# Optimization experiments

Hardware: AMD Instinct MI355X
Metric: run time of the kernel (lower is better)

Reference implementation:

```python
import jax, jax.numpy as jnp
import numpy as np

DIM = 1024
HEADS = 16
HEAD_DIM = DIM // HEADS


def setup_inputs() -> dict:
    key = jax.random.key(0)
    k_x, k_qkv, k_ow, k_ob = jax.random.split(key, 4)
    x = jax.random.normal(k_x, (2, 2048, DIM), dtype=jnp.float32)
    # nn.Linear(dim, 3*dim, bias=False): weight shape [3*dim, dim], y = x @ W.T
    w_qkv = jax.random.normal(k_qkv, (3 * DIM, DIM), dtype=jnp.float32) * (DIM ** -0.5)
    # nn.Linear(dim, dim) with bias
    w_o = jax.random.normal(k_ow, (DIM, DIM), dtype=jnp.float32) * (DIM ** -0.5)
    b_o = jax.random.normal(k_ob, (DIM,), dtype=jnp.float32) * 0.02
    return {"x": x, "w_qkv": w_qkv, "w_o": w_o, "b_o": b_o}


def reference(x, w_qkv, w_o, b_o):
    b, n, _ = x.shape
    scale = DIM ** -0.5  # NOTE: source scales by full dim, not head dim
    # qkv projection: [b, n, 3*dim]
    qkv = jnp.einsum('bnd,ed->bne', x, w_qkv)
    # 'b n (qkv h d) -> qkv b h n d'
    qkv = qkv.reshape(b, n, 3, HEADS, HEAD_DIM)
    q = jnp.transpose(qkv[:, :, 0], (0, 2, 1, 3))  # [b, h, n, d]
    k = jnp.transpose(qkv[:, :, 1], (0, 2, 1, 3))
    v = jnp.transpose(qkv[:, :, 2], (0, 2, 1, 3))
    scores = jnp.einsum('bhqd,bhkd->bhqk', q, k) * scale  # [b, h, n, n]
    attn = jax.nn.softmax(scores, axis=-1)
    out = jnp.einsum('bhqk,bhkd->bhqd', attn, v)  # [b, h, n, d]
    out = jnp.transpose(out, (0, 2, 1, 3)).reshape(b, n, DIM)  # 'b h n d -> b n (h d)'
    out = jnp.einsum('bnd,ed->bne', out, w_o) + b_o
    return out
```

## Files before the change

### kernel.cpp

```cpp
#include <hip/hip_runtime.h>
#include <stdint.h>


#define DIM 1024
#define SEQ 2048
#define BATCH 2
#define ROWS 4096
#define RSTRIDE 3072

typedef __bf16 bf16_t;
typedef bf16_t bf16x4 __attribute__((ext_vector_type(4)));
typedef bf16_t bf16x8 __attribute__((ext_vector_type(8)));
typedef float f32x4 __attribute__((ext_vector_type(4)));
typedef short s16x4 __attribute__((ext_vector_type(4)));

__device__ __forceinline__ ushort f2bf(float f) {
    uint32_t u;
    __builtin_memcpy(&u, &f, 4);
    uint32_t r = (u + 0x7fffu + ((u >> 16) & 1u)) >> 16;
    return (ushort)r;
}

__device__ __forceinline__ void store_out(ushort* p, float v) { *p = f2bf(v); }
__device__ __forceinline__ void store_out(float* p, float v) { *p = v; }

__device__ __forceinline__ void gl_lds16(const void* g, void* l) {
    __builtin_amdgcn_global_load_lds(
        (const __attribute__((address_space(1))) void*)g,
        (__attribute__((address_space(3))) void*)l, 16, 0, 0);
}

__global__ __launch_bounds__(256) void cvt3_kernel(
    const float* __restrict__ x, const float* __restrict__ wq,
    const float* __restrict__ wo, ushort* __restrict__ dst) {
    size_t i = ((size_t)blockIdx.x * 256 + threadIdx.x) * 8;
    const size_t n_x = (size_t)ROWS * DIM;
    const size_t n_wq = (size_t)3 * DIM * DIM;
    const float* src;
    size_t off;
    if (i < n_x) {
        src = x; off = i;
    } else if (i < n_x + n_wq) {
        src = wq; off = i - n_x;
    } else {
        src = wo; off = i - n_x - n_wq;
    }
    float4 a = *(const float4*)(src + off);
    float4 b = *(const float4*)(src + off + 4);
    uint4 u;
    u.x = (uint)f2bf(a.x) | ((uint)f2bf(a.y) << 16);
    u.y = (uint)f2bf(a.z) | ((uint)f2bf(a.w) << 16);
    u.z = (uint)f2bf(b.x) | ((uint)f2bf(b.y) << 16);
    u.w = (uint)f2bf(b.z) | ((uint)f2bf(b.w) << 16);
    *(uint4*)(dst + i) = u;
}

template <typename OutT, int BN>
__global__ __launch_bounds__(256) void gemm_bt_kernel(
    const ushort* __restrict__ A, const ushort* __restrict__ B,
    const float* __restrict__ bias, OutT* __restrict__ C,
    int M, int N, int K) {
    constexpr int JN = BN / 32;
    __shared__ __align__(16) ushort sA[128 * 64];
    __shared__ __align__(16) ushort sB[BN * 64];

    const int tid = threadIdx.x;
    const int lane = tid & 63, w = tid >> 6;
    const int quad = lane >> 4, l15 = lane & 15;
    const int wm = (w >> 1) * 64, wn = (w & 1) * (BN / 2);
    const int bm = blockIdx.y, bn = blockIdx.x;

    f32x4 acc[4][JN];
#pragma unroll
    for (int i = 0; i < 4; i++)
#pragma unroll
        for (int j = 0; j < JN; j++) acc[i][j] = (f32x4){0.f, 0.f, 0.f, 0.f};

    const ushort* Abase = A + (size_t)(bm * 128) * K;
    const ushort* Bbase = B + (size_t)(bn * BN) * K;
    const int rd = lane >> 3, c8 = lane & 7;
    const int sw = l15 & 7;

    for (int kk = 0; kk < K; kk += 64) {
        __syncthreads();
#pragma unroll
        for (int t = 0; t < 4; t++) {
            int row = w * 32 + t * 8;
            gl_lds16(Abase + (size_t)(row + rd) * K + kk + ((c8 ^ rd) * 8),
                     sA + row * 64);
        }
#pragma unroll
        for (int t = 0; t < BN / 32; t++) {
            int row = w * 8 + t * 32;
            gl_lds16(Bbase + (size_t)(row + rd) * K + kk + ((c8 ^ rd) * 8),
                     sB + row * 64);
        }
        __syncthreads();

#pragma unroll
        for (int kh = 0; kh < 2; kh++) {
            bf16x8 af[4], bfr[JN];
#pragma unroll
            for (int i = 0; i < 4; i++)
                af[i] = *(const bf16x8*)((const bf16_t*)sA +
                        (wm + i * 16 + l15) * 64 + (((kh * 4 + quad) ^ sw) * 8));
#pragma unroll
            for (int j = 0; j < JN; j++)
                bfr[j] = *(const bf16x8*)((const bf16_t*)sB +
                        (wn + j * 16 + l15) * 64 + (((kh * 4 + quad) ^ sw) * 8));
#pragma unroll
            for (int i = 0; i < 4; i++)
#pragma unroll
                for (int j = 0; j < JN; j++)
                    acc[i][j] = __builtin_amdgcn_mfma_f32_16x16x32_bf16(
                        af[i], bfr[j], acc[i][j], 0, 0, 0);
        }
    }

#pragma unroll
    for (int i = 0; i < 4; i++)
#pragma unroll
        for (int j = 0; j < JN; j++) {
            int col = bn * BN + wn + j * 16 + l15;
            float bv = bias ? bias[col] : 0.f;
#pragma unroll
            for (int r = 0; r < 4; r++) {
                int row = bm * 128 + wm + i * 16 + quad * 4 + r;
                store_out(&C[(size_t)row * N + col], acc[i][j][r] + bv);
            }
        }
}

template <typename OutT>
__global__ __launch_bounds__(512) void gemm_bt8_kernel(
    const ushort* __restrict__ A, const ushort* __restrict__ B,
    const float* __restrict__ bias, OutT* __restrict__ C,
    int M, int N, int K) {
    __shared__ __align__(16) ushort sA[128 * 64];
    __shared__ __align__(16) ushort sB[128 * 64];

    const int tid = threadIdx.x;
    const int lane = tid & 63, w = tid >> 6;
    const int quad = lane >> 4, l15 = lane & 15;
    const int wm = (w >> 2) * 64, wn = (w & 3) * 32;
    const int bm = blockIdx.y, bn = blockIdx.x;

    f32x4 acc[4][2];
#pragma unroll
    for (int i = 0; i < 4; i++)
#pragma unroll
        for (int j = 0; j < 2; j++) acc[i][j] = (f32x4){0.f, 0.f, 0.f, 0.f};

    const ushort* Abase = A + (size_t)(bm * 128) * K;
    const ushort* Bbase = B + (size_t)(bn * 128) * K;
    const int rd = lane >> 3, c8 = lane & 7;
    const int sw = l15 & 7;

    for (int kk = 0; kk < K; kk += 64) {
        __syncthreads();
#pragma unroll
        for (int t = 0; t < 2; t++) {
            int row = w * 16 + t * 8;
            gl_lds16(Abase + (size_t)(row + rd) * K + kk + ((c8 ^ rd) * 8),
                     sA + row * 64);
            gl_lds16(Bbase + (size_t)(row + rd) * K + kk + ((c8 ^ rd) * 8),
                     sB + row * 64);
        }
        __syncthreads();

#pragma unroll
        for (int kh = 0; kh < 2; kh++) {
            bf16x8 af[4], bfr[2];
#pragma unroll
            for (int i = 0; i < 4; i++)
                af[i] = *(const bf16x8*)((const bf16_t*)sA +
                        (wm + i * 16 + l15) * 64 + (((kh * 4 + quad) ^ sw) * 8));
#pragma unroll
            for (int j = 0; j < 2; j++)
                bfr[j] = *(const bf16x8*)((const bf16_t*)sB +
                        (wn + j * 16 + l15) * 64 + (((kh * 4 + quad) ^ sw) * 8));
#pragma unroll
            for (int i = 0; i < 4; i++)
#pragma unroll
                for (int j = 0; j < 2; j++)
                    acc[i][j] = __builtin_amdgcn_mfma_f32_16x16x32_bf16(
                        af[i], bfr[j], acc[i][j], 0, 0, 0);
        }
    }

#pragma unroll
    for (int i = 0; i < 4; i++)
#pragma unroll
        for (int j = 0; j < 2; j++) {
            int col = bn * 128 + wn + j * 16 + l15;
            float bv = bias ? bias[col] : 0.f;
#pragma unroll
            for (int r = 0; r < 4; r++) {
                int row = bm * 128 + wm + i * 16 + quad * 4 + r;
                store_out(&C[(size_t)row * N + col], acc[i][j][r] + bv);
            }
        }
}

__global__ __launch_bounds__(512, 4) void flash_attn_kernel(
    const ushort* __restrict__ qkv, ushort* __restrict__ out) {
    __shared__ __align__(16) ushort sK[128 * 64];
    __shared__ __align__(16) ushort sVt[64 * 128];

    const int tid = threadIdx.x;
    const int lane = tid & 63, w = tid >> 6;
    const int quad = lane >> 4, l15 = lane & 15;
    const int sw = l15 & 7;
    const int qh = quad >> 1, q1 = quad & 1;
    const int bh = blockIdx.y, b = bh >> 4, h = bh & 15;
    const int q0 = blockIdx.x * 128;
    const ushort* qkvb = qkv + (size_t)b * SEQ * RSTRIDE + h * 64;

    const ushort* qrow = qkvb + (size_t)(q0 + w * 16 + l15) * RSTRIDE;
    const bf16x8 aq0 = *(const bf16x8*)(qrow + quad * 8);
    const bf16x8 aq1 = *(const bf16x8*)(qrow + 32 + quad * 8);

    const int krow = tid >> 3, kc8 = tid & 7;
    const int kdst = krow * 64 + ((kc8 ^ (krow & 7)) * 8);
    const int vrp = tid & 63, vc = tid >> 6;
    const int vch = vrp >> 2, vlo = vrp & 3;

    uint4 kreg0, kreg1, va, vb;
    {
        const ushort* kp0 = qkvb + (size_t)krow * RSTRIDE + DIM + kc8 * 8;
        kreg0 = *(const uint4*)kp0;
        kreg1 = *(const uint4*)(kp0 + (size_t)64 * RSTRIDE);
        const ushort* v0 = qkvb + (size_t)(2 * vrp) * RSTRIDE + 2 * DIM + vc * 8;
        va = *(const uint4*)v0;
        vb = *(const uint4*)(v0 + RSTRIDE);
    }

    f32x4 l_acc = (f32x4){0.f, 0.f, 0.f, 0.f};
    f32x4 o[4];
#pragma unroll
    for (int j = 0; j < 4; j++) o[j] = (f32x4){0.f, 0.f, 0.f, 0.f};

    s16x4 vones;
#pragma unroll
    for (int e = 0; e < 4; e++) vones[e] = (short)0x3F80;

    const float c_exp = 0.04508422f;

    uint* vt32 = (uint*)sVt;
    for (int kb = 0; kb < SEQ; kb += 128) {
        *(uint4*)(sK + kdst) = kreg0;
        *(uint4*)(sK + 64 * 64 + kdst) = kreg1;
        {
            int base = (vc * 8) * 64 + vlo;
            vt32[base + 0 * 64 + ((vch ^ 0) << 2)] = (va.x & 0xffffu) | (vb.x << 16);
            vt32[base + 1 * 64 + ((vch ^ 1) << 2)] = (va.x >> 16) | (vb.x & 0xffff0000u);
            vt32[base + 2 * 64 + ((vch ^ 2) << 2)] = (va.y & 0xffffu) | (vb.y << 16);
            vt32[base + 3 * 64 + ((vch ^ 3) << 2)] = (va.y >> 16) | (vb.y & 0xffff0000u);
            vt32[base + 4 * 64 + ((vch ^ 4) << 2)] = (va.z & 0xffffu) | (vb.z << 16);
            vt32[base + 5 * 64 + ((vch ^ 5) << 2)] = (va.z >> 16) | (vb.z & 0xffff0000u);
            vt32[base + 6 * 64 + ((vch ^ 6) << 2)] = (va.w & 0xffffu) | (vb.w << 16);
            vt32[base + 7 * 64 + ((vch ^ 7) << 2)] = (va.w >> 16) | (vb.w & 0xffff0000u);
        }
        __syncthreads();

        int nkb = (kb + 128 < SEQ) ? kb + 128 : kb;
        {
            const ushort* kp0 = qkvb + (size_t)(nkb + krow) * RSTRIDE + DIM + kc8 * 8;
            kreg0 = *(const uint4*)kp0;
            kreg1 = *(const uint4*)(kp0 + (size_t)64 * RSTRIDE);
            const ushort* v0 =
                qkvb + (size_t)(nkb + 2 * vrp) * RSTRIDE + 2 * DIM + vc * 8;
            va = *(const uint4*)v0;
            vb = *(const uint4*)(v0 + RSTRIDE);
        }

        f32x4 s[8];
#pragma unroll
        for (int j = 0; j < 8; j++) {
            const ushort* kp = sK + (j * 16 + l15) * 64;
            bf16x8 bk0 = *(const bf16x8*)(kp + ((quad ^ sw) * 8));
            bf16x8 bk1 = *(const bf16x8*)(kp + (((4 | quad) ^ sw) * 8));
            f32x4 z = (f32x4){0.f, 0.f, 0.f, 0.f};
            __builtin_amdgcn_s_setprio(1);
            z = __builtin_amdgcn_mfma_f32_16x16x32_bf16(bk0, aq0, z, 0, 0, 0);
            z = __builtin_amdgcn_mfma_f32_16x16x32_bf16(bk1, aq1, z, 0, 0, 0);
            __builtin_amdgcn_s_setprio(0);
            s[j] = z;
        }

        s16x4 pa[8];
#pragma unroll
        for (int j = 0; j < 8; j++) {
            bf16x4 t;
#pragma unroll
            for (int r = 0; r < 4; r++)
                t[r] = (bf16_t)__builtin_amdgcn_exp2f(s[j][r] * c_exp);
            pa[j] = __builtin_bit_cast(s16x4, t);
        }

        __builtin_amdgcn_s_setprio(1);
#pragma unroll
        for (int j = 0; j < 8; j++)
            l_acc = __builtin_amdgcn_mfma_f32_16x16x16bf16_1k(
                pa[j], vones, l_acc, 0, 0, 0);
        __builtin_amdgcn_s_setprio(0);

#pragma unroll
        for (int jd = 0; jd < 4; jd++) {
            const bf16_t* vp = (const bf16_t*)sVt + (jd * 16 + l15) * 128;
            __builtin_amdgcn_s_setprio(1);
#pragma unroll
            for (int j = 0; j < 8; j++) {
                int ch = 2 * j + qh;
                bf16x4 bv = *(const bf16x4*)(vp + ((ch ^ sw) * 8 + q1 * 4));
                o[jd] = __builtin_amdgcn_mfma_f32_16x16x16bf16_1k(
                    pa[j], __builtin_bit_cast(s16x4, bv), o[jd], 0, 0, 0);
            }
            __builtin_amdgcn_s_setprio(0);
        }
        __syncthreads();
    }

#pragma unroll
    for (int r = 0; r < 4; r++) {
        float inv = 1.f / l_acc[r];
        int qrow_i = q0 + w * 16 + quad * 4 + r;
#pragma unroll
        for (int j = 0; j < 4; j++) {
            out[(size_t)(b * SEQ + qrow_i) * DIM + h * 64 + j * 16 + l15] =
                f2bf(o[j][r] * inv);
        }
    }
}

extern "C" void kernel_launch(void* const* d_in, const int* in_sizes, int n_in,
                              void* d_out, int out_size, void* d_ws, size_t ws_size,
                              hipStream_t stream) {
    const float* x = (const float*)d_in[0];
    const float* w_qkv = (const float*)d_in[1];
    const float* w_o = (const float*)d_in[2];
    const float* b_o = (const float*)d_in[3];
    float* out = (float*)d_out;

    ushort* qkv = (ushort*)d_ws;
    ushort* attn = qkv + (size_t)ROWS * 3 * DIM;
    ushort* xb = attn + (size_t)ROWS * DIM;
    ushort* wqkvb = xb + (size_t)ROWS * DIM;
    ushort* wob = wqkvb + (size_t)3 * DIM * DIM;

    dim3 blk(256);
    cvt3_kernel<<<(ROWS * DIM + 3 * DIM * DIM + DIM * DIM) / 2048, blk, 0,
                  stream>>>(x, w_qkv, w_o, xb);

    gemm_bt8_kernel<ushort>
        <<<dim3(3 * DIM / 128, ROWS / 128), dim3(512), 0, stream>>>(
            xb, wqkvb, nullptr, qkv, ROWS, 3 * DIM, DIM);
    flash_attn_kernel<<<dim3(SEQ / 128, BATCH * 16), dim3(512), 0, stream>>>(qkv, attn);
    gemm_bt_kernel<float, 64>
        <<<dim3(DIM / 64, ROWS / 128), blk, 0, stream>>>(
            attn, wob, b_o, out, ROWS, DIM, DIM);
}
```

Baseline: 188.1 us.

## Double-buffer GEMM LDS tiles and swizzle workgroups across XCDs

Both GEMM kernels now use two LDS buffers, issuing the global-to-LDS loads for the next K tile before computing on the current one, with a single barrier per iteration. This aims to hide global load latency behind the MFMA work. Workgroup indices in the GEMMs and flash attention are also remapped so that consecutive tiles land on the same XCD, which should improve L2 reuse. The cost is double the LDS per GEMM block, which may lower occupancy, plus a redundant final prefetch. The mapping also assumes grid sizes divisible by 8.

```diff
diff --git a/kernel.cpp b/kernel.cpp
--- a/kernel.cpp
+++ b/kernel.cpp
@@ -55,20 +55,26 @@
     *(uint4*)(dst + i) = u;
 }
 
+__device__ __forceinline__ int xcd_swz(int lin, int nwg) {
+    return (lin & 7) * (nwg >> 3) + (lin >> 3);
+}
+
 template <typename OutT, int BN>
 __global__ __launch_bounds__(256) void gemm_bt_kernel(
     const ushort* __restrict__ A, const ushort* __restrict__ B,
     const float* __restrict__ bias, OutT* __restrict__ C,
     int M, int N, int K) {
     constexpr int JN = BN / 32;
-    __shared__ __align__(16) ushort sA[128 * 64];
-    __shared__ __align__(16) ushort sB[BN * 64];
+    __shared__ __align__(16) ushort sA[2][128 * 64];
+    __shared__ __align__(16) ushort sB[2][BN * 64];
 
     const int tid = threadIdx.x;
     const int lane = tid & 63, w = tid >> 6;
     const int quad = lane >> 4, l15 = lane & 15;
     const int wm = (w >> 1) * 64, wn = (w & 1) * (BN / 2);
-    const int bm = blockIdx.y, bn = blockIdx.x;
+    const int lin = blockIdx.y * gridDim.x + blockIdx.x;
+    const int swz = xcd_swz(lin, gridDim.x * gridDim.y);
+    const int bm = swz / gridDim.x, bn = swz % gridDim.x;
 
     f32x4 acc[4][JN];
 #pragma unroll
@@ -81,32 +87,39 @@
     const int rd = lane >> 3, c8 = lane & 7;
     const int sw = l15 & 7;
 
-    for (int kk = 0; kk < K; kk += 64) {
-        __syncthreads();
-#pragma unroll
-        for (int t = 0; t < 4; t++) {
-            int row = w * 32 + t * 8;
-            gl_lds16(Abase + (size_t)(row + rd) * K + kk + ((c8 ^ rd) * 8),
-                     sA + row * 64);
-        }
-#pragma unroll
-        for (int t = 0; t < BN / 32; t++) {
-            int row = w * 8 + t * 32;
-            gl_lds16(Bbase + (size_t)(row + rd) * K + kk + ((c8 ^ rd) * 8),
-                     sB + row * 64);
-        }
-        __syncthreads();
+#define STAGE_G(buf, kk)                                                       \
+    do {                                                                       \
+        _Pragma("unroll") for (int t = 0; t < 4; t++) {                        \
+            int row = w * 32 + t * 8;                                          \
+            gl_lds16(Abase + (size_t)(row + rd) * K + (kk) + ((c8 ^ rd) * 8),  \
+                     &sA[buf][row * 64]);                                      \
+        }                                                                      \
+        _Pragma("unroll") for (int t = 0; t < BN / 32; t++) {                  \
+            int row = w * 8 + t * 32;                                          \
+            gl_lds16(Bbase + (size_t)(row + rd) * K + (kk) + ((c8 ^ rd) * 8),  \
+                     &sB[buf][row * 64]);                                      \
+        }                                                                      \
+    } while (0)
+
+    const int nsteps = K >> 6;
+    STAGE_G(0, 0);
+    __syncthreads();
+
+    for (int t = 0; t < nsteps; ++t) {
+        const int cur = t & 1;
+        int nkk = (t + 1 < nsteps) ? ((t + 1) << 6) : 0;
+        STAGE_G(cur ^ 1, nkk);
 
 #pragma unroll
         for (int kh = 0; kh < 2; kh++) {
             bf16x8 af[4], bfr[JN];
 #pragma unroll
             for (int i = 0; i < 4; i++)
-                af[i] = *(const bf16x8*)((const bf16_t*)sA +
+                af[i] = *(const bf16x8*)((const bf16_t*)sA[cur] +
                         (wm + i * 16 + l15) * 64 + (((kh * 4 + quad) ^ sw) * 8));
 #pragma unroll
             for (int j = 0; j < JN; j++)
-                bfr[j] = *(const bf16x8*)((const bf16_t*)sB +
+                bfr[j] = *(const bf16x8*)((const bf16_t*)sB[cur] +
                         (wn + j * 16 + l15) * 64 + (((kh * 4 + quad) ^ sw) * 8));
 #pragma unroll
             for (int i = 0; i < 4; i++)
@@ -115,7 +128,9 @@
                     acc[i][j] = __builtin_amdgcn_mfma_f32_16x16x32_bf16(
                         af[i], bfr[j], acc[i][j], 0, 0, 0);
         }
-    }
+        __syncthreads();
+    }
+#undef STAGE_G
 
 #pragma unroll
     for (int i = 0; i < 4; i++)
@@ -136,14 +151,16 @@
     const ushort* __restrict__ A, const ushort* __restrict__ B,
     const float* __restrict__ bias, OutT* __restrict__ C,
     int M, int N, int K) {
-    __shared__ __align__(16) ushort sA[128 * 64];
-    __shared__ __align__(16) ushort sB[128 * 64];
+    __shared__ __align__(16) ushort sA[2][128 * 64];
+    __shared__ __align__(16) ushort sB[2][128 * 64];
 
     const int tid = threadIdx.x;
     const int lane = tid & 63, w = tid >> 6;
     const int quad = lane >> 4, l15 = lane & 15;
     const int wm = (w >> 2) * 64, wn = (w & 3) * 32;
-    const int bm = blockIdx.y, bn = blockIdx.x;
+    const int lin = blockIdx.y * gridDim.x + blockIdx.x;
+    const int swz = xcd_swz(lin, gridDim.x * gridDim.y);
+    const int bm = swz / gridDim.x, bn = swz % gridDim.x;
 
     f32x4 acc[4][2];
 #pragma unroll
@@ -156,28 +173,36 @@
     const int rd = lane >> 3, c8 = lane & 7;
     const int sw = l15 & 7;
 
-    for (int kk = 0; kk < K; kk += 64) {
-        __syncthreads();
-#pragma unroll
-        for (int t = 0; t < 2; t++) {
-            int row = w * 16 + t * 8;
-            gl_lds16(Abase + (size_t)(row + rd) * K + kk + ((c8 ^ rd) * 8),
-                     sA + row * 64);
-            gl_lds16(Bbase + (size_t)(row + rd) * K + kk + ((c8 ^ rd) * 8),
-                     sB + row * 64);
-        }
-        __syncthreads();
+#define STAGE_G8(buf, kk)                                                      \
+    do {                                                                       \
+        _Pragma("unroll") for (int t = 0; t < 2; t++) {                        \
+            int row = w * 16 + t * 8;                                          \
+            gl_lds16(Abase + (size_t)(row + rd) * K + (kk) + ((c8 ^ rd) * 8),  \
+                     &sA[buf][row * 64]);                                      \
+            gl_lds16(Bbase + (size_t)(row + rd) * K + (kk) + ((c8 ^ rd) * 8),  \
+                     &sB[buf][row * 64]);                                      \
+        }                                                                      \
+    } while (0)
+
+    const int nsteps = K >> 6;
+    STAGE_G8(0, 0);
+    __syncthreads();
+
+    for (int t = 0; t < nsteps; ++t) {
+        const int cur = t & 1;
+        int nkk = (t + 1 < nsteps) ? ((t + 1) << 6) : 0;
+        STAGE_G8(cur ^ 1, nkk);
 
 #pragma unroll
         for (int kh = 0; kh < 2; kh++) {
             bf16x8 af[4], bfr[2];
 #pragma unroll
             for (int i = 0; i < 4; i++)
-                af[i] = *(const bf16x8*)((const bf16_t*)sA +
+                af[i] = *(const bf16x8*)((const bf16_t*)sA[cur] +
                         (wm + i * 16 + l15) * 64 + (((kh * 4 + quad) ^ sw) * 8));
 #pragma unroll
             for (int j = 0; j < 2; j++)
-                bfr[j] = *(const bf16x8*)((const bf16_t*)sB +
+                bfr[j] = *(const bf16x8*)((const bf16_t*)sB[cur] +
                         (wn + j * 16 + l15) * 64 + (((kh * 4 + quad) ^ sw) * 8));
 #pragma unroll
             for (int i = 0; i < 4; i++)
@@ -186,7 +211,9 @@
                     acc[i][j] = __builtin_amdgcn_mfma_f32_16x16x32_bf16(
                         af[i], bfr[j], acc[i][j], 0, 0, 0);
         }
-    }
+        __syncthreads();
+    }
+#undef STAGE_G8
 
 #pragma unroll
     for (int i = 0; i < 4; i++)
@@ -212,8 +239,10 @@
     const int quad = lane >> 4, l15 = lane & 15;
     const int sw = l15 & 7;
     const int qh = quad >> 1, q1 = quad & 1;
-    const int bh = blockIdx.y, b = bh >> 4, h = bh & 15;
-    const int q0 = blockIdx.x * 128;
+    const int lin = blockIdx.y * gridDim.x + blockIdx.x;
+    const int swzb = xcd_swz(lin, 512);
+    const int bh = swzb >> 4, b = bh >> 4, h = bh & 15;
+    const int q0 = (swzb & 15) * 128;
     const ushort* qkvb = qkv + (size_t)b * SEQ * RSTRIDE + h * 64;
 
     const ushort* qrow = qkvb + (size_t)(q0 + w * 16 + l15) * RSTRIDE;
```

Measured after the change: 195.9 us. +4.2%, slower.

## Add XCD-aware block swizzling to GEMMs and attention, double-buffer output GEMM

Applied to the files above, without the earlier changes.

Remaps linear block IDs so that blocks landing on the same XCD (round-robin over 8) work on neighbouring tiles, improving L2 reuse in the QKV GEMM, the attention kernel and the output projection. The QKV GEMM moves to the 256-thread BN=128 kernel with a grouped 8x12 tile mapping per XCD. The output projection uses a new double-buffered LDS variant that prefetches the next K slice while the current one computes. In exchange, LDS use doubles for that kernel and the QKV GEMM goes from 8 waves per block to 4.

```diff
diff --git a/kernel.cpp b/kernel.cpp
--- a/kernel.cpp
+++ b/kernel.cpp
@@ -55,7 +55,11 @@
     *(uint4*)(dst + i) = u;
 }
 
-template <typename OutT, int BN>
+__device__ __forceinline__ int xcd_swz(int lin, int nwg) {
+    return (lin & 7) * (nwg >> 3) + (lin >> 3);
+}
+
+template <typename OutT, int BN, int CR, int CC>
 __global__ __launch_bounds__(256) void gemm_bt_kernel(
     const ushort* __restrict__ A, const ushort* __restrict__ B,
     const float* __restrict__ bias, OutT* __restrict__ C,
@@ -68,7 +72,18 @@
     const int lane = tid & 63, w = tid >> 6;
     const int quad = lane >> 4, l15 = lane & 15;
     const int wm = (w >> 1) * 64, wn = (w & 1) * (BN / 2);
-    const int bm = blockIdx.y, bn = blockIdx.x;
+    const int lin = blockIdx.y * gridDim.x + blockIdx.x;
+    int bm, bn;
+    if constexpr (CR > 0) {
+        int xcd = lin & 7, idx = lin >> 3;
+        int rcols = 24 / CC;
+        bm = (xcd / rcols) * CR + idx / CC;
+        bn = (xcd % rcols) * CC + idx % CC;
+    } else {
+        int swz = xcd_swz(lin, gridDim.x * gridDim.y);
+        bm = swz / gridDim.x;
+        bn = swz % gridDim.x;
+    }
 
     f32x4 acc[4][JN];
 #pragma unroll
@@ -131,68 +146,85 @@
         }
 }
 
-template <typename OutT>
-__global__ __launch_bounds__(512) void gemm_bt8_kernel(
+template <typename OutT, int BN>
+__global__ __launch_bounds__(256) void gemm_bt_db_kernel(
     const ushort* __restrict__ A, const ushort* __restrict__ B,
     const float* __restrict__ bias, OutT* __restrict__ C,
     int M, int N, int K) {
-    __shared__ __align__(16) ushort sA[128 * 64];
-    __shared__ __align__(16) ushort sB[128 * 64];
+    constexpr int JN = BN / 32;
+    __shared__ __align__(16) ushort sA[2][128 * 64];
+    __shared__ __align__(16) ushort sB[2][BN * 64];
 
     const int tid = threadIdx.x;
     const int lane = tid & 63, w = tid >> 6;
     const int quad = lane >> 4, l15 = lane & 15;
-    const int wm = (w >> 2) * 64, wn = (w & 3) * 32;
-    const int bm = blockIdx.y, bn = blockIdx.x;
-
-    f32x4 acc[4][2];
+    const int wm = (w >> 1) * 64, wn = (w & 1) * (BN / 2);
+    const int lin = blockIdx.y * gridDim.x + blockIdx.x;
+    const int swz = xcd_swz(lin, gridDim.x * gridDim.y);
+    const int bm = swz / gridDim.x, bn = swz % gridDim.x;
+
+    f32x4 acc[4][JN];
 #pragma unroll
     for (int i = 0; i < 4; i++)
 #pragma unroll
-        for (int j = 0; j < 2; j++) acc[i][j] = (f32x4){0.f, 0.f, 0.f, 0.f};
+        for (int j = 0; j < JN; j++) acc[i][j] = (f32x4){0.f, 0.f, 0.f, 0.f};
 
     const ushort* Abase = A + (size_t)(bm * 128) * K;
-    const ushort* Bbase = B + (size_t)(bn * 128) * K;
+    const ushort* Bbase = B + (size_t)(bn * BN) * K;
     const int rd = lane >> 3, c8 = lane & 7;
     const int sw = l15 & 7;
 
-    for (int kk = 0; kk < K; kk += 64) {
-        __syncthreads();
-#pragma unroll
-        for (int t = 0; t < 2; t++) {
-            int row = w * 16 + t * 8;
-            gl_lds16(Abase + (size_t)(row + rd) * K + kk + ((c8 ^ rd) * 8),
-                     sA + row * 64);
-            gl_lds16(Bbase + (size_t)(row + rd) * K + kk + ((c8 ^ rd) * 8),
-                     sB + row * 64);
-        }
-        __syncthreads();
+#define STAGE_DB(buf, kkof)                                                    \
+    do {                                                                       \
+        _Pragma("unroll") for (int tt = 0; tt < 4; tt++) {                     \
+            int row = w * 32 + tt * 8;                                         \
+            gl_lds16(Abase + (size_t)(row + rd) * K + (kkof) + ((c8 ^ rd) * 8),\
+                     &sA[buf][row * 64]);                                      \
+        }                                                                      \
+        _Pragma("unroll") for (int tt = 0; tt < BN / 32; tt++) {               \
+            int row = w * 8 + tt * 32;                                         \
+            gl_lds16(Bbase + (size_t)(row + rd) * K + (kkof) + ((c8 ^ rd) * 8),\
+                     &sB[buf][row * 64]);                                      \
+        }                                                                      \
+    } while (0)
+
+    const int nsteps = K >> 6;
+    STAGE_DB(0, 0);
+    __syncthreads();
+
+    for (int t = 0; t < nsteps; ++t) {
+        const int cur = t & 1;
+        const int nxt = cur ^ 1;
+        const int nk = (t + 1) << 6;
+        if (t + 1 < nsteps) STAGE_DB(nxt, nk);
 
 #pragma unroll
         for (int kh = 0; kh < 2; kh++) {
-            bf16x8 af[4], bfr[2];
+            bf16x8 af[4], bfr[JN];
 #pragma unroll
             for (int i = 0; i < 4; i++)
-                af[i] = *(const bf16x8*)((const bf16_t*)sA +
+                af[i] = *(const bf16x8*)((const bf16_t*)sA[cur] +
                         (wm + i * 16 + l15) * 64 + (((kh * 4 + quad) ^ sw) * 8));
 #pragma unroll
-            for (int j = 0; j < 2; j++)
-                bfr[j] = *(const bf16x8*)((const bf16_t*)sB +
+            for (int j = 0; j < JN; j++)
+                bfr[j] = *(const bf16x8*)((const bf16_t*)sB[cur] +
                         (wn + j * 16 + l15) * 64 + (((kh * 4 + quad) ^ sw) * 8));
 #pragma unroll
             for (int i = 0; i < 4; i++)
 #pragma unroll
-                for (int j = 0; j < 2; j++)
+                for (int j = 0; j < JN; j++)
                     acc[i][j] = __builtin_amdgcn_mfma_f32_16x16x32_bf16(
                         af[i], bfr[j], acc[i][j], 0, 0, 0);
         }
-    }
+        __syncthreads();
+    }
+#undef STAGE_DB
 
 #pragma unroll
     for (int i = 0; i < 4; i++)
 #pragma unroll
-        for (int j = 0; j < 2; j++) {
-            int col = bn * 128 + wn + j * 16 + l15;
+        for (int j = 0; j < JN; j++) {
+            int col = bn * BN + wn + j * 16 + l15;
             float bv = bias ? bias[col] : 0.f;
 #pragma unroll
             for (int r = 0; r < 4; r++) {
@@ -212,8 +244,10 @@
     const int quad = lane >> 4, l15 = lane & 15;
     const int sw = l15 & 7;
     const int qh = quad >> 1, q1 = quad & 1;
-    const int bh = blockIdx.y, b = bh >> 4, h = bh & 15;
-    const int q0 = blockIdx.x * 128;
+    const int lin = blockIdx.y * gridDim.x + blockIdx.x;
+    const int swzb = xcd_swz(lin, 512);
+    const int bh = swzb >> 4, b = bh >> 4, h = bh & 15;
+    const int q0 = (swzb & 15) * 128;
     const ushort* qkvb = qkv + (size_t)b * SEQ * RSTRIDE + h * 64;
 
     const ushort* qrow = qkvb + (size_t)(q0 + w * 16 + l15) * RSTRIDE;
@@ -352,11 +386,11 @@
     cvt3_kernel<<<(ROWS * DIM + 3 * DIM * DIM + DIM * DIM) / 2048, blk, 0,
                   stream>>>(x, w_qkv, w_o, xb);
 
-    gemm_bt8_kernel<ushort>
-        <<<dim3(3 * DIM / 128, ROWS / 128), dim3(512), 0, stream>>>(
+    gemm_bt_kernel<ushort, 128, 8, 12>
+        <<<dim3(3 * DIM / 128, ROWS / 128), blk, 0, stream>>>(
             xb, wqkvb, nullptr, qkv, ROWS, 3 * DIM, DIM);
     flash_attn_kernel<<<dim3(SEQ / 128, BATCH * 16), dim3(512), 0, stream>>>(qkv, attn);
-    gemm_bt_kernel<float, 64>
+    gemm_bt_db_kernel<float, 64>
         <<<dim3(DIM / 64, ROWS / 128), blk, 0, stream>>>(
             attn, wob, b_o, out, ROWS, DIM, DIM);
 }
```

After: 184.3 us. 2.0% less time.
